# Performance work log

Measured on AMD Instinct MI355X. Metric: run time of the kernel, lower is better.

Reference implementation:

```python
import jax, jax.numpy as jnp
import numpy as np

SOS = 0
MAX_LENGTH = 64

N_LATENTS = 256
N_CHARACTERS = 128
N_HIDDENS = 1024
BATCH = 4096


def setup_inputs() -> dict:
    key = jax.random.key(0)
    ks = jax.random.split(key, 16)
    H, L, C = N_HIDDENS, N_LATENTS, N_CHARACTERS
    s = 0.02
    return {
        "z": jax.random.normal(ks[0], (BATCH, L), dtype=jnp.float32),
        "embed_w": jax.random.normal(ks[1], (C, H), dtype=jnp.float32) * s,
        "z2h_w": jax.random.normal(ks[2], (H, L), dtype=jnp.float32) * s,
        "z2h_b": jnp.zeros((H,), dtype=jnp.float32),
        "w_ih0": jax.random.normal(ks[3], (3 * H, H + L), dtype=jnp.float32) * s,
        "w_hh0": jax.random.normal(ks[4], (3 * H, H), dtype=jnp.float32) * s,
        "b_ih0": jnp.zeros((3 * H,), dtype=jnp.float32),
        "b_hh0": jnp.zeros((3 * H,), dtype=jnp.float32),
        "w_ih1": jax.random.normal(ks[5], (3 * H, H), dtype=jnp.float32) * s,
        "w_hh1": jax.random.normal(ks[6], (3 * H, H), dtype=jnp.float32) * s,
        "b_ih1": jnp.zeros((3 * H,), dtype=jnp.float32),
        "b_hh1": jnp.zeros((3 * H,), dtype=jnp.float32),
        "h2o_w": jax.random.normal(ks[7], (C, H + L), dtype=jnp.float32) * s,
        "h2o_b": jnp.zeros((C,), dtype=jnp.float32),
    }


def _gru_cell(x, h, w_ih, w_hh, b_ih, b_hh):
    # PyTorch GRUCell math. x: [B, I], h: [B, H]
    gi = x @ w_ih.T + b_ih  # [B, 3H]
    gh = h @ w_hh.T + b_hh  # [B, 3H]
    i_r, i_z, i_n = jnp.split(gi, 3, axis=1)
    h_r, h_z, h_n = jnp.split(gh, 3, axis=1)
    r = jax.nn.sigmoid(i_r + h_r)
    zg = jax.nn.sigmoid(i_z + h_z)
    n = jnp.tanh(i_n + r * h_n)
    return (1.0 - zg) * n + zg * h


def reference(z, embed_w, z2h_w, z2h_b,
              w_ih0, w_hh0, b_ih0, b_hh0,
              w_ih1, w_hh1, b_ih1, b_hh1,
              h2o_w, h2o_b):
    batch = z.shape[0]
    h0 = z @ z2h_w.T + z2h_b  # [B, H], replicated across both GRU layers

    def step(carry, _):
        c_in, h1, h2 = carry
        e = embed_w[c_in]                      # [B, H] embedding lookup
        e = e * jax.nn.sigmoid(e)              # swish
        x = jnp.concatenate([e, z], axis=1)    # [B, H+L]
        h1 = _gru_cell(x, h1, w_ih0, w_hh0, b_ih0, b_hh0)
        h2 = _gru_cell(h1, h2, w_ih1, w_hh1, b_ih1, b_hh1)
        out = jnp.concatenate([h2, z], axis=1) @ h2o_w.T + h2o_b  # [B, C]
        # argmax(log_softmax(out)) == argmax(out)
        sample = jnp.argmax(out, axis=1).astype(jnp.int32)
        return (sample, h1, h2), out

    c0 = jnp.full((batch,), SOS, dtype=jnp.int32)
    _, outs = jax.lax.scan(step, (c0, h0, h0), None, length=MAX_LENGTH)
    return jnp.transpose(outs, (1, 0, 2))  # [B, T, C]
```

## Files before the change

### kernel.cpp

```cpp
#include <hip/hip_runtime.h>
#include <hip/hip_bf16.h>
#include <stdint.h>
#include <stddef.h>

#define B_   4096
#define H_   1024
#define L_   256
#define C_   128
#define T_   64
#define H3_  3072

typedef unsigned short u16;
typedef __attribute__((ext_vector_type(8))) short bf16x8;
typedef __attribute__((ext_vector_type(4))) float f32x4;

typedef const void __attribute__((address_space(1)))* as1_cvp;
typedef void __attribute__((address_space(3)))* as3_vp;

__device__ __forceinline__ void gl2lds16(const void* g, void* l) {
  __builtin_amdgcn_global_load_lds((as1_cvp)g, (as3_vp)l, 16, 0, 0);
}

__device__ __forceinline__ float bf2f(u16 u) {
  union { float f; unsigned int i; } x; x.i = ((unsigned int)u) << 16; return x.f;
}
__device__ __forceinline__ u16 f2bf(float f) {
  union { float f; unsigned int i; } x; x.f = f;
  unsigned int r = x.i + 0x7fffu + ((x.i >> 16) & 1u);
  return (u16)(r >> 16);
}
__device__ __forceinline__ float sigm(float x) { return 1.f / (1.f + __expf(-x)); }
__device__ __forceinline__ float tanh_fast(float x) {
  float e = __expf(2.f * x); return 1.f - 2.f / (e + 1.f);
}

template<int OUT_MODE>
__device__ __forceinline__ void gemm_tile_body(
    u16* As, u16* Ws,
    const u16* __restrict__ A, int lda,
    const u16* __restrict__ W, int ldw,
    const float* __restrict__ bias,
    void* __restrict__ C0p, void* __restrict__ C1p, int ldc, int K,
    int m0, int n0)
{
  const int tid  = threadIdx.x;
  const int wave = tid >> 6, lane = tid & 63;
  const int wm = (wave >> 1) * 64, wn = (wave & 1) * 64;
  const int lrow = lane & 15, lq = lane >> 4;
  const int arow = wave * 8 + (lane >> 3);
  const int acol = (lane & 7) * 8;

  f32x4 acc[4][4] = {};

  const u16* Ag = A + (size_t)m0 * lda;
  const u16* Wg = W + (size_t)n0 * ldw;

  for (int k0 = 0; k0 < K; k0 += 64) {
    __syncthreads();
    #pragma unroll
    for (int rd = 0; rd < 4; rd++) {
      gl2lds16(Ag + (size_t)(rd * 32 + arow) * lda + (k0 + acol), As + rd * 2048 + wave * 512);
      gl2lds16(Wg + (size_t)(rd * 32 + arow) * ldw + (k0 + acol), Ws + rd * 2048 + wave * 512);
    }
    __syncthreads();
    #pragma unroll
    for (int kk = 0; kk < 64; kk += 32) {
      bf16x8 af[4], bw[4];
      #pragma unroll
      for (int i = 0; i < 4; i++)
        af[i] = *(const bf16x8*)&As[(wm + i * 16 + lrow) * 64 + kk + lq * 8];
      #pragma unroll
      for (int j = 0; j < 4; j++)
        bw[j] = *(const bf16x8*)&Ws[(wn + j * 16 + lrow) * 64 + kk + lq * 8];
      #pragma unroll
      for (int i = 0; i < 4; i++)
        #pragma unroll
        for (int j = 0; j < 4; j++)
          acc[i][j] = __builtin_amdgcn_mfma_f32_16x16x32_bf16(af[i], bw[j], acc[i][j], 0, 0, 0);
    }
  }

  #pragma unroll
  for (int j = 0; j < 4; j++) {
    const int col = n0 + wn + j * 16 + lrow;
    const float bv = bias ? bias[col] : 0.f;
    #pragma unroll
    for (int i = 0; i < 4; i++) {
      #pragma unroll
      for (int r = 0; r < 4; r++) {
        const int row = m0 + wm + i * 16 + lq * 4 + r;
        float v = acc[i][j][r] + bv;
        if (OUT_MODE == 0) {
          ((float*)C0p)[(size_t)row * ldc + col] = v;
        } else if (OUT_MODE == 1) {
          ((u16*)C0p)[(size_t)row * ldc + col] = f2bf(v);
        } else {
          u16 hv = f2bf(v);
          ((u16*)C0p)[(size_t)row * ldc + col] = hv;
          ((u16*)C1p)[(size_t)row * ldc + col] = hv;
        }
      }
    }
  }
}

template<int OUT_MODE>
__global__ __launch_bounds__(256) void gemm_bt(
    const u16* __restrict__ A, int lda,
    const u16* __restrict__ W, int ldw,
    const float* __restrict__ bias,
    void* __restrict__ C0p, void* __restrict__ C1p, int ldc, int K)
{
  __shared__ __align__(16) u16 As[128 * 64];
  __shared__ __align__(16) u16 Ws[128 * 64];
  gemm_tile_body<OUT_MODE>(As, Ws, A, lda, W, ldw, bias, C0p, C1p, ldc, K,
                           blockIdx.y * 128, blockIdx.x * 128);
}

__device__ __forceinline__ void out_body(
    u16* As, u16* Ws, int ob,
    const u16* __restrict__ h2, const u16* __restrict__ Wo,
    const float* __restrict__ Oz, float* __restrict__ outp,
    int* __restrict__ cnew, int t)
{
  const int tid = threadIdx.x, wave = tid >> 6, lane = tid & 63;
  const int b0 = ob * 64;
  const int lrow = lane & 15, lq = lane >> 4;
  const int arow = wave * 8 + (lane >> 3);
  const int acol = (lane & 7) * 8;
  f32x4 acc[8] = {};

  for (int k0 = 0; k0 < H_; k0 += 64) {
    __syncthreads();
    #pragma unroll
    for (int rd = 0; rd < 2; rd++)
      gl2lds16(h2 + (size_t)(b0 + rd * 32 + arow) * H_ + k0 + acol, As + rd * 2048 + wave * 512);
    #pragma unroll
    for (int rd = 0; rd < 4; rd++)
      gl2lds16(Wo + (size_t)(rd * 32 + arow) * H_ + k0 + acol, Ws + rd * 2048 + wave * 512);
    __syncthreads();
    #pragma unroll
    for (int kk = 0; kk < 64; kk += 32) {
      bf16x8 af = *(const bf16x8*)&As[(wave * 16 + lrow) * 64 + kk + lq * 8];
      #pragma unroll
      for (int j = 0; j < 8; j++) {
        bf16x8 bw = *(const bf16x8*)&Ws[(j * 16 + lrow) * 64 + kk + lq * 8];
        acc[j] = __builtin_amdgcn_mfma_f32_16x16x32_bf16(af, bw, acc[j], 0, 0, 0);
      }
    }
  }

  #pragma unroll
  for (int r = 0; r < 4; r++) {
    const int row = b0 + wave * 16 + lq * 4 + r;
    float mv = -3.4e38f; int mi = 0;
    #pragma unroll
    for (int j = 0; j < 8; j++) {
      const int col = j * 16 + lrow;
      float v = acc[j][r] + Oz[(size_t)row * C_ + col];
      outp[(size_t)row * (T_ * C_) + t * C_ + col] = v;
      if (v > mv) { mv = v; mi = col; }
    }
    #pragma unroll
    for (int off = 1; off < 16; off <<= 1) {
      float ov = __shfl_xor(mv, off);
      int   oi = __shfl_xor(mi, off);
      if (ov > mv || (ov == mv && oi < mi)) { mv = ov; mi = oi; }
    }
    if (lrow == 0) cnew[row] = mi;
  }
}

__global__ __launch_bounds__(256) void step1(
    const u16* __restrict__ h1, const u16* __restrict__ whh0,
    const float* __restrict__ b_hh0, u16* __restrict__ gh0,
    const u16* __restrict__ h2cur, const u16* __restrict__ Wo,
    const float* __restrict__ Oz, float* __restrict__ outp,
    int* __restrict__ cbuf, int tprev)
{
  __shared__ __align__(16) u16 As[128 * 64];
  __shared__ __align__(16) u16 Ws[128 * 64];
  int bid = blockIdx.x;
  if (bid < 64) {
    if (tprev >= 0) out_body(As, Ws, bid, h2cur, Wo, Oz, outp, cbuf, tprev);
    return;
  }
  const int g = bid - 64;
  const int xcd = g & 7, k = g >> 3;
  const int n = xcd * 3 + (k % 3);
  const int m = k / 3;
  gemm_tile_body<1>(As, Ws, h1, H_, whh0, H_, b_hh0, gh0, nullptr, H3_, H_,
                    m * 128, n * 128);
}

template<bool PH2>
__device__ __forceinline__ void l3_phase(
    u16* As, u16* Ws,
    const u16* __restrict__ Ag, const u16* __restrict__ Wg, int j0,
    f32x4 acc[3][2][4], f32x4 accN[2][4])
{
  const int tid = threadIdx.x, wave = tid >> 6, lane = tid & 63;
  const int wmh = wave >> 1, wj = wave & 1;
  const int lrow = lane & 15, lq = lane >> 4;
  const int arow = wave * 8 + (lane >> 3);
  const int acol = (lane & 7) * 8;

  for (int k0 = 0; k0 < H_; k0 += 64) {
    __syncthreads();
    #pragma unroll
    for (int rd = 0; rd < 4; rd++)
      gl2lds16(Ag + (size_t)(rd * 32 + arow) * H_ + (k0 + acol), As + rd * 2048 + wave * 512);
    #pragma unroll
    for (int rd = 0; rd < 6; rd++)
      gl2lds16(Wg + (size_t)((rd >> 1) * 1024 + j0 + (rd & 1) * 32 + arow) * H_ + (k0 + acol),
               Ws + rd * 2048 + wave * 512);
    __syncthreads();
    #pragma unroll
    for (int kk = 0; kk < 64; kk += 32) {
      bf16x8 af[4];
      #pragma unroll
      for (int i = 0; i < 4; i++)
        af[i] = *(const bf16x8*)&As[(wmh * 64 + i * 16 + lrow) * 64 + kk + lq * 8];
      #pragma unroll
      for (int g = 0; g < 3; g++) {
        #pragma unroll
        for (int u = 0; u < 2; u++) {
          bf16x8 bw = *(const bf16x8*)&Ws[(g * 64 + wj * 32 + u * 16 + lrow) * 64 + kk + lq * 8];
          #pragma unroll
          for (int i = 0; i < 4; i++) {
            if (PH2 && g == 2)
              accN[u][i] = __builtin_amdgcn_mfma_f32_16x16x32_bf16(af[i], bw, accN[u][i], 0, 0, 0);
            else
              acc[g][u][i] = __builtin_amdgcn_mfma_f32_16x16x32_bf16(af[i], bw, acc[g][u][i], 0, 0, 0);
          }
        }
      }
    }
  }
}

__global__ __launch_bounds__(256, 2) void gemm_l3(
    const u16* __restrict__ h1, const u16* __restrict__ h2old,
    const u16* __restrict__ wih1, const u16* __restrict__ whh1,
    const float* __restrict__ b_ih1, const float* __restrict__ b_hh1,
    u16* __restrict__ h2new)
{
  __shared__ __align__(16) u16 As[128 * 64];
  __shared__ __align__(16) u16 Ws[192 * 64];
  const int bid = blockIdx.x;
  const int xcd = bid & 7, k = bid >> 3;
  const int jt = xcd * 2 + (k & 1);
  const int m  = k >> 1;
  const int m0 = m * 128, j0 = jt * 64;

  f32x4 acc[3][2][4] = {};
  f32x4 accN[2][4] = {};

  l3_phase<false>(As, Ws, h1    + (size_t)m0 * H_, wih1, j0, acc, accN);
  l3_phase<true >(As, Ws, h2old + (size_t)m0 * H_, whh1, j0, acc, accN);

  const int tid = threadIdx.x, wave = tid >> 6, lane = tid & 63;
  const int wmh = wave >> 1, wj = wave & 1;
  const int lrow = lane & 15, lq = lane >> 4;

  #pragma unroll
  for (int u = 0; u < 2; u++) {
    const int j = j0 + wj * 32 + u * 16 + lrow;
    const float bR  = b_ih1[j] + b_hh1[j];
    const float bZ  = b_ih1[H_ + j] + b_hh1[H_ + j];
    const float bNi = b_ih1[2 * H_ + j];
    const float bNh = b_hh1[2 * H_ + j];
    #pragma unroll
    for (int i = 0; i < 4; i++) {
      #pragma unroll
      for (int rr = 0; rr < 4; rr++) {
        const int row = m0 + wmh * 64 + i * 16 + lq * 4 + rr;
        float r  = sigm(acc[0][u][i][rr] + bR);
        float zg = sigm(acc[1][u][i][rr] + bZ);
        float nn = tanh_fast(acc[2][u][i][rr] + bNi + r * (accN[u][i][rr] + bNh));
        float hold = bf2f(h2old[(size_t)row * H_ + j]);
        h2new[(size_t)row * H_ + j] = f2bf((1.f - zg) * nn + zg * hold);
      }
    }
  }
}

__global__ __launch_bounds__(256) void gru_cell0_v(
    const int* __restrict__ c, const u16* __restrict__ Egi,
    const u16* __restrict__ Gz, const u16* __restrict__ gh,
    u16* __restrict__ h1)
{
  const int b = blockIdx.x, j = threadIdx.x * 4;
  const u16* eg = Egi + (size_t)c[b] * H3_ + j;
  const size_t g = (size_t)b * H3_ + j;
  ushort4 er = *(const ushort4*)&eg[0];
  ushort4 ez = *(const ushort4*)&eg[H_];
  ushort4 en = *(const ushort4*)&eg[2 * H_];
  ushort4 zr = *(const ushort4*)&Gz[g];
  ushort4 zz = *(const ushort4*)&Gz[g + H_];
  ushort4 zn = *(const ushort4*)&Gz[g + 2 * H_];
  ushort4 hr = *(const ushort4*)&gh[g];
  ushort4 hz = *(const ushort4*)&gh[g + H_];
  ushort4 hn = *(const ushort4*)&gh[g + 2 * H_];
  const size_t hi = (size_t)b * H_ + j;
  ushort4 hold = *(const ushort4*)&h1[hi];
  ushort4 outv;
  #pragma unroll
  for (int k = 0; k < 4; k++) {
    float gir = bf2f(((const u16*)&er)[k]) + bf2f(((const u16*)&zr)[k]);
    float giz = bf2f(((const u16*)&ez)[k]) + bf2f(((const u16*)&zz)[k]);
    float gin = bf2f(((const u16*)&en)[k]) + bf2f(((const u16*)&zn)[k]);
    float r  = sigm(gir + bf2f(((const u16*)&hr)[k]));
    float zg = sigm(giz + bf2f(((const u16*)&hz)[k]));
    float nn = tanh_fast(gin + r * bf2f(((const u16*)&hn)[k]));
    float h = bf2f(((const u16*)&hold)[k]);
    ((u16*)&outv)[k] = f2bf((1.f - zg) * nn + zg * h);
  }
  *(ushort4*)&h1[hi] = outv;
}

__global__ __launch_bounds__(256) void conv_bf16_k(const float* __restrict__ s, u16* __restrict__ d, int n) {
  int i = blockIdx.x * 256 + threadIdx.x;
  if (i < n) d[i] = f2bf(s[i]);
}
__global__ __launch_bounds__(256) void conv_split_k(const float* __restrict__ s, u16* __restrict__ dA,
                                                    u16* __restrict__ dZ, int rows) {
  int i = blockIdx.x * 256 + threadIdx.x;
  if (i >= rows * 1280) return;
  int rr = i / 1280, col = i - rr * 1280;
  float v = s[i];
  if (col < 1024) dA[(size_t)rr * 1024 + col] = f2bf(v);
  else            dZ[(size_t)rr * 256 + (col - 1024)] = f2bf(v);
}
__global__ __launch_bounds__(256) void conv_swish_k(const float* __restrict__ s, u16* __restrict__ d, int n) {
  int i = blockIdx.x * 256 + threadIdx.x;
  if (i < n) { float e = s[i]; d[i] = f2bf(e * sigm(e)); }
}

static inline char* wsal(char*& p, size_t bytes) {
  char* r = p; p += (bytes + 255) & ~(size_t)255; return r;
}

extern "C" void kernel_launch(void* const* d_in, const int* in_sizes, int n_in,
                              void* d_out, int out_size, void* d_ws, size_t ws_size,
                              hipStream_t stream) {
  const float* z       = (const float*)d_in[0];
  const float* embed_w = (const float*)d_in[1];
  const float* z2h_w   = (const float*)d_in[2];
  const float* z2h_b   = (const float*)d_in[3];
  const float* w_ih0   = (const float*)d_in[4];
  const float* w_hh0   = (const float*)d_in[5];
  const float* b_ih0   = (const float*)d_in[6];
  const float* b_hh0   = (const float*)d_in[7];
  const float* w_ih1   = (const float*)d_in[8];
  const float* w_hh1   = (const float*)d_in[9];
  const float* b_ih1   = (const float*)d_in[10];
  const float* b_hh1   = (const float*)d_in[11];
  const float* h2o_w   = (const float*)d_in[12];
  const float* h2o_b   = (const float*)d_in[13];
  float* outp = (float*)d_out;

  char* p = (char*)d_ws;
  u16* whh0  = (u16*)wsal(p, (size_t)H3_ * H_ * 2);
  u16* wih1  = (u16*)wsal(p, (size_t)H3_ * H_ * 2);
  u16* whh1  = (u16*)wsal(p, (size_t)H3_ * H_ * 2);
  u16* wih0a = (u16*)wsal(p, (size_t)H3_ * H_ * 2);
  u16* wih0z = (u16*)wsal(p, (size_t)H3_ * L_ * 2);
  u16* h2oa  = (u16*)wsal(p, (size_t)C_ * H_ * 2);
  u16* h2oz  = (u16*)wsal(p, (size_t)C_ * L_ * 2);
  u16* z2hb  = (u16*)wsal(p, (size_t)H_ * L_ * 2);
  u16* zb    = (u16*)wsal(p, (size_t)B_ * L_ * 2);
  u16* swe   = (u16*)wsal(p, (size_t)C_ * H_ * 2);
  u16* EgiB  = (u16*)wsal(p, (size_t)C_ * H3_ * 2);
  u16* Gz    = (u16*)wsal(p, (size_t)B_ * H3_ * 2);
  float* Oz  = (float*)wsal(p, (size_t)B_ * C_ * 4);
  u16* h1    = (u16*)wsal(p, (size_t)B_ * H_ * 2);
  u16* h2a   = (u16*)wsal(p, (size_t)B_ * H_ * 2);
  u16* h2b   = (u16*)wsal(p, (size_t)B_ * H_ * 2);
  u16* gh0   = (u16*)wsal(p, (size_t)B_ * H3_ * 2);
  int* cbuf  = (int*)wsal(p, (size_t)B_ * 4);

  conv_bf16_k<<<(B_*L_ + 255)/256, 256, 0, stream>>>(z, zb, B_*L_);
  conv_bf16_k<<<(H_*L_ + 255)/256, 256, 0, stream>>>(z2h_w, z2hb, H_*L_);
  conv_bf16_k<<<(H3_*H_ + 255)/256, 256, 0, stream>>>(w_hh0, whh0, H3_*H_);
  conv_bf16_k<<<(H3_*H_ + 255)/256, 256, 0, stream>>>(w_ih1, wih1, H3_*H_);
  conv_bf16_k<<<(H3_*H_ + 255)/256, 256, 0, stream>>>(w_hh1, whh1, H3_*H_);
  conv_split_k<<<(H3_*1280 + 255)/256, 256, 0, stream>>>(w_ih0, wih0a, wih0z, H3_);
  conv_split_k<<<(C_*1280 + 255)/256, 256, 0, stream>>>(h2o_w, h2oa, h2oz, C_);
  conv_swish_k<<<(C_*H_ + 255)/256, 256, 0, stream>>>(embed_w, swe, C_*H_);
  hipMemsetAsync(cbuf, 0, B_ * sizeof(int), stream);

  gemm_bt<2><<<dim3(H_/128, B_/128), 256, 0, stream>>>(zb, L_, z2hb, L_, z2h_b, h1, h2a, H_, L_);
  gemm_bt<1><<<dim3(H3_/128, 1), 256, 0, stream>>>(swe, H_, wih0a, H_, b_ih0, EgiB, nullptr, H3_, H_);
  gemm_bt<1><<<dim3(H3_/128, B_/128), 256, 0, stream>>>(zb, L_, wih0z, L_, nullptr, Gz, nullptr, H3_, L_);
  gemm_bt<0><<<dim3(1, B_/128), 256, 0, stream>>>(zb, L_, h2oz, L_, h2o_b, Oz, nullptr, C_, L_);

  for (int t = 0; t < T_; t++) {
    const u16* h2cur = (t & 1) ? h2b : h2a;
    u16*       h2nxt = (t & 1) ? h2a : h2b;
    step1<<<832, 256, 0, stream>>>(h1, whh0, b_hh0, gh0, h2cur, h2oa, Oz, outp, cbuf, t - 1);
    gru_cell0_v<<<B_, 256, 0, stream>>>(cbuf, EgiB, Gz, gh0, h1);
    gemm_l3<<<512, 256, 0, stream>>>(h1, h2cur, wih1, whh1, b_ih1, b_hh1, h2nxt);
  }
  step1<<<64, 256, 0, stream>>>(h1, whh0, b_hh0, gh0, h2a, h2oa, Oz, outp, cbuf, T_ - 1);
}
```

Before: 8.396 ms.

## Fuse layer-0 GRU cell into hidden GEMM epilogue and split output kernel

Replaces the generic gh0 GEMM plus separate elementwise GRU cell kernel with a gate-grouped GEMM (reusing the l3_phase layout) that applies the GRU nonlinearity in its epilogue. The epilogue gathers the embedding and z gate contributions directly. h1 is double-buffered so the old state can be read while the new one is written. The output projection moves into its own small kernel instead of sharing a launch with the hidden GEMM. This removes the gh0 intermediate round trip through memory and one launch per step. In exchange the output kernel is now serialized rather than co-scheduled, and the epilogue uses scalar scattered loads.

New measurement: 8.450 ms. Within noise of the previous version (+0.6%).

```diff
diff --git a/kernel.cpp b/kernel.cpp
--- a/kernel.cpp
+++ b/kernel.cpp
@@ -171,26 +171,14 @@
   }
 }
 
-__global__ __launch_bounds__(256) void step1(
-    const u16* __restrict__ h1, const u16* __restrict__ whh0,
-    const float* __restrict__ b_hh0, u16* __restrict__ gh0,
+__global__ __launch_bounds__(256) void out_k(
     const u16* __restrict__ h2cur, const u16* __restrict__ Wo,
     const float* __restrict__ Oz, float* __restrict__ outp,
-    int* __restrict__ cbuf, int tprev)
-{
-  __shared__ __align__(16) u16 As[128 * 64];
+    int* __restrict__ cbuf, int t)
+{
+  __shared__ __align__(16) u16 As[64 * 64];
   __shared__ __align__(16) u16 Ws[128 * 64];
-  int bid = blockIdx.x;
-  if (bid < 64) {
-    if (tprev >= 0) out_body(As, Ws, bid, h2cur, Wo, Oz, outp, cbuf, tprev);
-    return;
-  }
-  const int g = bid - 64;
-  const int xcd = g & 7, k = g >> 3;
-  const int n = xcd * 3 + (k % 3);
-  const int m = k / 3;
-  gemm_tile_body<1>(As, Ws, h1, H_, whh0, H_, b_hh0, gh0, nullptr, H3_, H_,
-                    m * 128, n * 128);
+  out_body(As, Ws, blockIdx.x, h2cur, Wo, Oz, outp, cbuf, t);
 }
 
 template<bool PH2>
@@ -239,6 +227,53 @@
   }
 }
 
+__global__ __launch_bounds__(256, 2) void gemm_g1(
+    const u16* __restrict__ h1old, const u16* __restrict__ whh0,
+    const float* __restrict__ b_hh0,
+    const int* __restrict__ cbuf, const u16* __restrict__ Egi,
+    const u16* __restrict__ Gz, u16* __restrict__ h1new)
+{
+  __shared__ __align__(16) u16 As[128 * 64];
+  __shared__ __align__(16) u16 Ws[192 * 64];
+  const int bid = blockIdx.x;
+  const int xcd = bid & 7, k = bid >> 3;
+  const int jt = xcd * 2 + (k & 1);
+  const int m  = k >> 1;
+  const int m0 = m * 128, j0 = jt * 64;
+
+  f32x4 acc[3][2][4] = {};
+  f32x4 accN[2][4] = {};
+
+  l3_phase<false>(As, Ws, h1old + (size_t)m0 * H_, whh0, j0, acc, accN);
+
+  const int tid = threadIdx.x, wave = tid >> 6, lane = tid & 63;
+  const int wmh = wave >> 1, wj = wave & 1;
+  const int lrow = lane & 15, lq = lane >> 4;
+
+  #pragma unroll
+  for (int u = 0; u < 2; u++) {
+    const int j = j0 + wj * 32 + u * 16 + lrow;
+    const float bR = b_hh0[j];
+    const float bZ = b_hh0[H_ + j];
+    const float bN = b_hh0[2 * H_ + j];
+    #pragma unroll
+    for (int i = 0; i < 4; i++) {
+      #pragma unroll
+      for (int rr = 0; rr < 4; rr++) {
+        const int row = m0 + wmh * 64 + i * 16 + lq * 4 + rr;
+        const size_t eb = (size_t)cbuf[row] * H3_ + j;
+        const size_t gb = (size_t)row * H3_ + j;
+        float r  = sigm(bf2f(Egi[eb])           + bf2f(Gz[gb])           + acc[0][u][i][rr] + bR);
+        float zg = sigm(bf2f(Egi[eb + H_])      + bf2f(Gz[gb + H_])      + acc[1][u][i][rr] + bZ);
+        float nn = tanh_fast(bf2f(Egi[eb + 2 * H_]) + bf2f(Gz[gb + 2 * H_])
+                             + r * (acc[2][u][i][rr] + bN));
+        float hold = bf2f(h1old[(size_t)row * H_ + j]);
+        h1new[(size_t)row * H_ + j] = f2bf((1.f - zg) * nn + zg * hold);
+      }
+    }
+  }
+}
+
 __global__ __launch_bounds__(256, 2) void gemm_l3(
     const u16* __restrict__ h1, const u16* __restrict__ h2old,
     const u16* __restrict__ wih1, const u16* __restrict__ whh1,
@@ -283,40 +318,6 @@
       }
     }
   }
-}
-
-__global__ __launch_bounds__(256) void gru_cell0_v(
-    const int* __restrict__ c, const u16* __restrict__ Egi,
-    const u16* __restrict__ Gz, const u16* __restrict__ gh,
-    u16* __restrict__ h1)
-{
-  const int b = blockIdx.x, j = threadIdx.x * 4;
-  const u16* eg = Egi + (size_t)c[b] * H3_ + j;
-  const size_t g = (size_t)b * H3_ + j;
-  ushort4 er = *(const ushort4*)&eg[0];
-  ushort4 ez = *(const ushort4*)&eg[H_];
-  ushort4 en = *(const ushort4*)&eg[2 * H_];
-  ushort4 zr = *(const ushort4*)&Gz[g];
-  ushort4 zz = *(const ushort4*)&Gz[g + H_];
-  ushort4 zn = *(const ushort4*)&Gz[g + 2 * H_];
-  ushort4 hr = *(const ushort4*)&gh[g];
-  ushort4 hz = *(const ushort4*)&gh[g + H_];
-  ushort4 hn = *(const ushort4*)&gh[g + 2 * H_];
-  const size_t hi = (size_t)b * H_ + j;
-  ushort4 hold = *(const ushort4*)&h1[hi];
-  ushort4 outv;
-  #pragma unroll
-  for (int k = 0; k < 4; k++) {
-    float gir = bf2f(((const u16*)&er)[k]) + bf2f(((const u16*)&zr)[k]);
-    float giz = bf2f(((const u16*)&ez)[k]) + bf2f(((const u16*)&zz)[k]);
-    float gin = bf2f(((const u16*)&en)[k]) + bf2f(((const u16*)&zn)[k]);
-    float r  = sigm(gir + bf2f(((const u16*)&hr)[k]));
-    float zg = sigm(giz + bf2f(((const u16*)&hz)[k]));
-    float nn = tanh_fast(gin + r * bf2f(((const u16*)&hn)[k]));
-    float h = bf2f(((const u16*)&hold)[k]);
-    ((u16*)&outv)[k] = f2bf((1.f - zg) * nn + zg * h);
-  }
-  *(ushort4*)&h1[hi] = outv;
 }
 
 __global__ __launch_bounds__(256) void conv_bf16_k(const float* __restrict__ s, u16* __restrict__ d, int n) {
@@ -374,10 +375,10 @@
   u16* EgiB  = (u16*)wsal(p, (size_t)C_ * H3_ * 2);
   u16* Gz    = (u16*)wsal(p, (size_t)B_ * H3_ * 2);
   float* Oz  = (float*)wsal(p, (size_t)B_ * C_ * 4);
-  u16* h1    = (u16*)wsal(p, (size_t)B_ * H_ * 2);
+  u16* h1a   = (u16*)wsal(p, (size_t)B_ * H_ * 2);
+  u16* h1b   = (u16*)wsal(p, (size_t)B_ * H_ * 2);
   u16* h2a   = (u16*)wsal(p, (size_t)B_ * H_ * 2);
   u16* h2b   = (u16*)wsal(p, (size_t)B_ * H_ * 2);
-  u16* gh0   = (u16*)wsal(p, (size_t)B_ * H3_ * 2);
   int* cbuf  = (int*)wsal(p, (size_t)B_ * 4);
 
   conv_bf16_k<<<(B_*L_ + 255)/256, 256, 0, stream>>>(z, zb, B_*L_);
@@ -390,7 +391,7 @@
   conv_swish_k<<<(C_*H_ + 255)/256, 256, 0, stream>>>(embed_w, swe, C_*H_);
   hipMemsetAsync(cbuf, 0, B_ * sizeof(int), stream);
 
-  gemm_bt<2><<<dim3(H_/128, B_/128), 256, 0, stream>>>(zb, L_, z2hb, L_, z2h_b, h1, h2a, H_, L_);
+  gemm_bt<2><<<dim3(H_/128, B_/128), 256, 0, stream>>>(zb, L_, z2hb, L_, z2h_b, h1a, h2a, H_, L_);
   gemm_bt<1><<<dim3(H3_/128, 1), 256, 0, stream>>>(swe, H_, wih0a, H_, b_ih0, EgiB, nullptr, H3_, H_);
   gemm_bt<1><<<dim3(H3_/128, B_/128), 256, 0, stream>>>(zb, L_, wih0z, L_, nullptr, Gz, nullptr, H3_, L_);
   gemm_bt<0><<<dim3(1, B_/128), 256, 0, stream>>>(zb, L_, h2oz, L_, h2o_b, Oz, nullptr, C_, L_);
@@ -398,9 +399,12 @@
   for (int t = 0; t < T_; t++) {
     const u16* h2cur = (t & 1) ? h2b : h2a;
     u16*       h2nxt = (t & 1) ? h2a : h2b;
-    step1<<<832, 256, 0, stream>>>(h1, whh0, b_hh0, gh0, h2cur, h2oa, Oz, outp, cbuf, t - 1);
-    gru_cell0_v<<<B_, 256, 0, stream>>>(cbuf, EgiB, Gz, gh0, h1);
-    gemm_l3<<<512, 256, 0, stream>>>(h1, h2cur, wih1, whh1, b_ih1, b_hh1, h2nxt);
-  }
-  step1<<<64, 256, 0, stream>>>(h1, whh0, b_hh0, gh0, h2a, h2oa, Oz, outp, cbuf, T_ - 1);
-}
+    const u16* h1cur = (t & 1) ? h1b : h1a;
+    u16*       h1nxt = (t & 1) ? h1a : h1b;
+    if (t > 0)
+      out_k<<<64, 256, 0, stream>>>(h2cur, h2oa, Oz, outp, cbuf, t - 1);
+    gemm_g1<<<512, 256, 0, stream>>>(h1cur, whh0, b_hh0, cbuf, EgiB, Gz, h1nxt);
+    gemm_l3<<<512, 256, 0, stream>>>(h1nxt, h2cur, wih1, whh1, b_ih1, b_hh1, h2nxt);
+  }
+  out_k<<<64, 256, 0, stream>>>(h2a, h2oa, Oz, outp, cbuf, T_ - 1);
+}
```
